# Performance work log

Measured on AMD Instinct MI355X. Metric: run time of the kernel, lower is better.

## Reference

```python
import math
import jax, jax.numpy as jnp
import numpy as np

B, N, D, H, PREFIX = 2, 2048, 2048, 16, 512
HD = D // H
ROPE_BASE = 10000.0

def _rope(x):
    # x: [b, h, n, d]; rotate-half RoPE with positions 0..n-1
    d = x.shape[-1]
    n = x.shape[-2]
    inv_freq = 1.0 / (ROPE_BASE ** (jnp.arange(0, d, 2, dtype=jnp.float32) / d))  # [d/2]
    pos = jnp.arange(n, dtype=jnp.float32)
    freqs = pos[:, None] * inv_freq[None, :]            # [n, d/2]
    cos, sin = jnp.cos(freqs), jnp.sin(freqs)
    x1, x2 = x[..., : d // 2], x[..., d // 2 :]
    return jnp.concatenate([x1 * cos - x2 * sin, x2 * cos + x1 * sin], axis=-1).astype(x.dtype)

def setup_inputs() -> dict:
    key = jax.random.key(0)
    ks = jax.random.split(key, 6)
    x = jax.random.normal(ks[0], (B, N, D), dtype=jnp.float32)
    prefix_k = jax.random.normal(ks[1], (B, H, PREFIX, HD), dtype=jnp.float32)
    prefix_v = jax.random.normal(ks[2], (B, H, PREFIX, HD), dtype=jnp.float32)
    Wqkv = jax.random.normal(ks[3], (D, 3 * D), dtype=jnp.float32) * (D ** -0.5)
    bqkv = jnp.zeros((3 * D,), dtype=jnp.float32)
    Wff = jax.random.normal(ks[4], (D, D), dtype=jnp.float32) * (D ** -0.5)
    bff = jnp.zeros((D,), dtype=jnp.float32)
    # causal mask over current tokens; prefix (cache) columns fully visible
    causal = jnp.tril(jnp.ones((N, N), dtype=jnp.int32))
    mask = jnp.concatenate([jnp.ones((N, PREFIX), dtype=jnp.int32), causal], axis=1)[None, None]  # [1,1,N,N+PREFIX]
    return {"x": x, "mask": mask, "prefix_k": prefix_k, "prefix_v": prefix_v,
            "Wqkv": Wqkv, "bqkv": bqkv, "Wff": Wff, "bff": bff}

def reference(x, mask, prefix_k, prefix_v, Wqkv, bqkv, Wff, bff):
    b, n, d = x.shape
    h = prefix_k.shape[1]
    hd = d // h
    qkv = (x @ Wqkv + bqkv).reshape(b, n, 3, h, hd)      # 'b n (c h d)'
    qkv = jnp.transpose(qkv, (2, 0, 3, 1, 4))            # -> c b h n d
    q, k, v = qkv[0], qkv[1], qkv[2]
    k = jnp.concatenate([prefix_k, k], axis=2)           # [b,h,kt,hd]
    v = jnp.concatenate([prefix_v, v], axis=2)
    next_prefix_kv = jnp.stack([k, v])                   # cached BEFORE rope (as in source)
    q = _rope(q)
    k = _rope(k)
    scores = jnp.einsum('bhqd,bhkd->bhqk', q, k) / math.sqrt(hd)
    scores = jnp.where(mask == 0, jnp.finfo(scores.dtype).min, scores)
    probs = jax.nn.softmax(scores, axis=-1)              # dropout_prob=0.0 -> identity
    attn_o = jnp.einsum('bhqk,bhkd->bhqd', probs, v)
    attn_o = jnp.transpose(attn_o, (0, 2, 1, 3)).reshape(b, n, d)
    return attn_o @ Wff + bff, next_prefix_kv
```

## Files before the change

### kernel.cpp

```cpp
#include <hip/hip_runtime.h>
#include <hip/hip_bf16.h>
#include <stdint.h>

#define TPB 256

using f32x4 = __attribute__((ext_vector_type(4))) float;
using s16x8 = __attribute__((ext_vector_type(8))) short;
using s16x4 = __attribute__((ext_vector_type(4))) short;

__device__ __forceinline__ short f2bf(float f){
  union { float f; uint32_t u; } v; v.f = f;
  uint32_t u = v.u;
  uint32_t r = (u + 0x7fffu + ((u >> 16) & 1u)) >> 16;
  return (short)(uint16_t)r;
}
__device__ __forceinline__ float bf2f(short b){
  union { uint32_t u; float f; } v; v.u = ((uint32_t)(uint16_t)b) << 16;
  return v.f;
}
__device__ __forceinline__ f32x4 mfma16(s16x8 a, s16x8 b, f32x4 c){
  return __builtin_amdgcn_mfma_f32_16x16x32_bf16(a, b, c, 0, 0, 0);
}

#define AS1(p) ((const __attribute__((address_space(1))) void*)(p))
#define AS3(p) ((__attribute__((address_space(3))) void*)(p))

__device__ __forceinline__ void trans64(const float* __restrict__ W, short* __restrict__ WT,
                                        int K, int Nn, int kt, int nt,
                                        float (*ls)[68], int tid){
  const int k0 = kt*64, n0 = nt*64;
#pragma unroll
  for (int i = 0; i < 4; i++){
    const int row = i*16 + (tid >> 4);
    const int c4  = (tid & 15) * 4;
    float4 v = *(const float4*)&W[(size_t)(k0+row)*Nn + n0 + c4];
    ls[row][c4+0] = v.x; ls[row][c4+1] = v.y; ls[row][c4+2] = v.z; ls[row][c4+3] = v.w;
  }
  __syncthreads();
#pragma unroll
  for (int j = 0; j < 2; j++){
    const int nr = j*32 + (tid >> 3);
    const int kc = (tid & 7) * 8;
    s16x8 o;
#pragma unroll
    for (int e = 0; e < 8; e++) o[e] = f2bf(ls[kc+e][nr]);
    *(s16x8*)&WT[(size_t)(n0+nr)*K + k0 + kc] = o;
  }
}

__global__ void k_prep(const float* __restrict__ x, short* __restrict__ xb,
                       const float* __restrict__ Wqkv, short* __restrict__ wqkvT,
                       const float* __restrict__ Wff,  short* __restrict__ wffT){
  __shared__ float ls[64][68];
  const int tid = threadIdx.x;
  const int bid = (int)blockIdx.x;
  if (bid < 4096){
    int i = bid * TPB + tid;
    const float4* s4 = (const float4*)x;
    float4 a = s4[2*i], b = s4[2*i+1];
    s16x8 o;
    o[0]=f2bf(a.x); o[1]=f2bf(a.y); o[2]=f2bf(a.z); o[3]=f2bf(a.w);
    o[4]=f2bf(b.x); o[5]=f2bf(b.y); o[6]=f2bf(b.z); o[7]=f2bf(b.w);
    *(s16x8*)(xb + 8*(size_t)i) = o;
  } else if (bid < 7168){
    const int tb = bid - 4096;
    trans64(Wqkv, wqkvT, 2048, 6144, tb & 31, tb >> 5, ls, tid);
  } else {
    const int tb = bid - 7168;
    trans64(Wff, wffT, 2048, 2048, tb & 31, tb >> 5, ls, tid);
  }
}

template<int EPI>
__global__ void __launch_bounds__(512, 2) k_gemm8(
    const short* __restrict__ A, const short* __restrict__ Bt,
    int Nn, int K,
    const float* __restrict__ bias,
    float* __restrict__ outp,
    float* __restrict__ kvout,
    short* __restrict__ qpre, short* __restrict__ kpre, short* __restrict__ vpre)
{
  __shared__ __align__(16) short As[3][16384];
  __shared__ __align__(16) short Bs[3][8192];
  const int tid = threadIdx.x;
  const int w = tid >> 6, l = tid & 63;
  const int lrow = l & 15, lg = l >> 4;
  const int wm = w >> 1, wn = w & 1;
  const int m0 = blockIdx.x << 8, n0 = blockIdx.y << 7;
  const int NT = K >> 6;

  f32x4 acc[4][4] = {};

#define STAGE_A(slot, t, j) do {                                             \
    int chunk = ((w*4 + (j)) << 6) + l;                                      \
    int row = chunk >> 3, cc = chunk & 7;                                    \
    __builtin_amdgcn_global_load_lds(                                        \
      AS1(A + (size_t)(m0+row)*K + (t)*64 + ((cc ^ (row&7)) << 3)),          \
      AS3(&As[slot][(w*4 + (j)) << 9]), 16, 0, 0);                           \
  } while(0)
#define STAGE_B(slot, t, j) do {                                             \
    int chunk = ((w*2 + (j)) << 6) + l;                                      \
    int row = chunk >> 3, cc = chunk & 7;                                    \
    __builtin_amdgcn_global_load_lds(                                        \
      AS1(Bt + (size_t)(n0+row)*K + (t)*64 + ((cc ^ (row&7)) << 3)),         \
      AS3(&Bs[slot][(w*2 + (j)) << 9]), 16, 0, 0);                           \
  } while(0)

  STAGE_A(0,0,0); STAGE_A(0,0,1); STAGE_A(0,0,2); STAGE_A(0,0,3);
  STAGE_B(0,0,0); STAGE_B(0,0,1);
  STAGE_A(1,1,0); STAGE_A(1,1,1); STAGE_A(1,1,2); STAGE_A(1,1,3);
  STAGE_B(1,1,0); STAGE_B(1,1,1);

  int slot = 0;
  for (int t = 0; t < NT; ++t){
    if (t < NT-1) asm volatile("s_waitcnt vmcnt(6)" ::: "memory");
    else          asm volatile("s_waitcnt vmcnt(0)" ::: "memory");
    __builtin_amdgcn_s_barrier();
    asm volatile("" ::: "memory");
    const int sslot = (slot == 0) ? 2 : slot - 1;
    const bool st = (t+2) < NT;
    const char* ab = (const char*)As[slot];
    const char* bb = (const char*)Bs[slot];

    s16x8 bfr[4][2];
#pragma unroll
    for (int ni = 0; ni < 4; ni++){
      int row = wn*64 + ni*16 + lrow;
#pragma unroll
      for (int ks = 0; ks < 2; ks++)
        bfr[ni][ks] = *(const s16x8*)(bb + row*128 + ((ks*64 + lg*16) ^ ((row&7)<<4)));
    }
    s16x8 af[2][2];
#pragma unroll
    for (int mi = 0; mi < 2; mi++){
      int row = wm*64 + mi*16 + lrow;
#pragma unroll
      for (int ks = 0; ks < 2; ks++)
        af[mi][ks] = *(const s16x8*)(ab + row*128 + ((ks*64 + lg*16) ^ ((row&7)<<4)));
    }
    if (st){ STAGE_A(sslot,t+2,0); STAGE_A(sslot,t+2,1); STAGE_B(sslot,t+2,0); }
    __builtin_amdgcn_s_setprio(1);
#pragma unroll
    for (int ks = 0; ks < 2; ks++)
#pragma unroll
      for (int mi = 0; mi < 2; mi++)
#pragma unroll
        for (int ni = 0; ni < 4; ni++)
          acc[mi][ni] = mfma16(af[mi][ks], bfr[ni][ks], acc[mi][ni]);
    __builtin_amdgcn_s_setprio(0);

    s16x8 af2[2][2];
#pragma unroll
    for (int mi = 0; mi < 2; mi++){
      int row = wm*64 + (mi+2)*16 + lrow;
#pragma unroll
      for (int ks = 0; ks < 2; ks++)
        af2[mi][ks] = *(const s16x8*)(ab + row*128 + ((ks*64 + lg*16) ^ ((row&7)<<4)));
    }
    if (st){ STAGE_A(sslot,t+2,2); STAGE_A(sslot,t+2,3); STAGE_B(sslot,t+2,1); }
    __builtin_amdgcn_s_setprio(1);
#pragma unroll
    for (int ks = 0; ks < 2; ks++)
#pragma unroll
      for (int mi = 0; mi < 2; mi++)
#pragma unroll
        for (int ni = 0; ni < 4; ni++)
          acc[mi+2][ni] = mfma16(af2[mi][ks], bfr[ni][ks], acc[mi+2][ni]);
    __builtin_amdgcn_s_setprio(0);
    slot = (slot == 2) ? 0 : slot + 1;
  }
#undef STAGE_A
#undef STAGE_B

#pragma unroll
  for (int mi = 0; mi < 4; mi++){
#pragma unroll
    for (int ni = 0; ni < 4; ni++){
      const int c  = n0 + wn*64 + ni*16 + lrow;
      const int mb = m0 + wm*64 + mi*16 + lg*4;
      const float bv = bias[c];
      if (EPI == 1){
#pragma unroll
        for (int r = 0; r < 4; r++)
          outp[(size_t)(mb+r)*Nn + c] = acc[mi][ni][r] + bv;
      } else {
        const int s = c >> 11, h = (c >> 7) & 15, tt = c & 127;
#pragma unroll
        for (int r = 0; r < 4; r++){
          const int m = mb + r;
          const int b = m >> 11, n = m & 2047;
          const int bh = b*16 + h;
          const float val = acc[mi][ni][r] + bv;
          if (s == 0){
            qpre[((size_t)bh*2048 + n)*128 + tt] = f2bf(val);
          } else if (s == 1){
            kvout[((size_t)bh*2560 + 512 + n)*128 + tt] = val;
            kpre[((size_t)bh*2048 + n)*128 + tt] = f2bf(val);
          } else {
            kvout[(size_t)(32 + bh)*327680 + (size_t)(512 + n)*128 + tt] = val;
            vpre[((size_t)bh*2048 + n)*128 + tt] = f2bf(val);
          }
        }
      }
    }
  }
}

__global__ void k_pre(const short* __restrict__ kpre, short* __restrict__ kr,
                      const short* __restrict__ vpre, short* __restrict__ vT,
                      const float* __restrict__ pk, float* __restrict__ kvout0,
                      const float* __restrict__ pv, float* __restrict__ kvout1){
  __shared__ float ls[32][129];
  const int tid = threadIdx.x;
  const int bid = (int)blockIdx.x;
  if (bid < 2048){
    int gid = bid * TPB + tid;
    int jb = (gid & 7) * 8; size_t row = gid >> 3;
    int bh = (int)(row >> 11), n = (int)(row & 2047);
    int pos = 512 + n;
    s16x8 v1 = *(const s16x8*)&kpre[row*128 + jb];
    s16x8 v2 = *(const s16x8*)&kpre[row*128 + 64 + jb];
    s16x8 o1, o2;
#pragma unroll
    for (int e = 0; e < 8; e++){
      float invf = __expf((float)(jb + e) * (-9.210340371976184f/64.0f));
      float sn, cs; __sincosf((float)pos * invf, &sn, &cs);
      float x1 = bf2f(v1[e]), x2 = bf2f(v2[e]);
      o1[e] = f2bf(x1*cs - x2*sn);
      o2[e] = f2bf(x2*cs + x1*sn);
    }
    size_t drow = (size_t)bh*2560 + pos;
    *(s16x8*)&kr[drow*128 + jb]      = o1;
    *(s16x8*)&kr[drow*128 + 64 + jb] = o2;
  } else if (bid < 4096){
    int t2 = bid - 2048;
    int bh = t2 >> 6, nt = t2 & 63;
    int n0 = nt*32;
#pragma unroll
    for (int i = 0; i < 16; i++){
      int idx = i*TPB + tid; int p = idx >> 7, t = idx & 127;
      ls[p][t] = bf2f(vpre[((size_t)bh*2048 + n0 + p)*128 + t]);
    }
    __syncthreads();
#pragma unroll
    for (int i = 0; i < 16; i++){
      int idx = i*TPB + tid; int t = idx >> 5, p = idx & 31;
      vT[((size_t)bh*128 + t)*2560 + 512 + n0 + p] = f2bf(ls[p][t]);
    }
  } else if (bid < 4608){
    int gid = (bid - 4096) * TPB + tid;
    int jb = (gid & 7) * 8; size_t row = gid >> 3;
    int bh = (int)(row >> 9), p = (int)(row & 511);
    float4 a1 = *(const float4*)&pk[row*128 + jb];
    float4 a2 = *(const float4*)&pk[row*128 + jb + 4];
    float4 b1 = *(const float4*)&pk[row*128 + 64 + jb];
    float4 b2 = *(const float4*)&pk[row*128 + 64 + jb + 4];
    size_t orow = (size_t)bh*2560 + p;
    *(float4*)&kvout0[orow*128 + jb]          = a1;
    *(float4*)&kvout0[orow*128 + jb + 4]      = a2;
    *(float4*)&kvout0[orow*128 + 64 + jb]     = b1;
    *(float4*)&kvout0[orow*128 + 64 + jb + 4] = b2;
    float x1[8] = {a1.x,a1.y,a1.z,a1.w,a2.x,a2.y,a2.z,a2.w};
    float x2[8] = {b1.x,b1.y,b1.z,b1.w,b2.x,b2.y,b2.z,b2.w};
    s16x8 o1, o2;
#pragma unroll
    for (int e = 0; e < 8; e++){
      float invf = __expf((float)(jb + e) * (-9.210340371976184f/64.0f));
      float sn, cs; __sincosf((float)p * invf, &sn, &cs);
      o1[e] = f2bf(x1[e]*cs - x2[e]*sn);
      o2[e] = f2bf(x2[e]*cs + x1[e]*sn);
    }
    *(s16x8*)&kr[orow*128 + jb]      = o1;
    *(s16x8*)&kr[orow*128 + 64 + jb] = o2;
  } else {
    int t2 = bid - 4608;
    int bh = t2 >> 4, pt = t2 & 15;
    int p0 = pt*32;
#pragma unroll
    for (int i = 0; i < 16; i++){
      int idx = i*TPB + tid; int p = idx >> 7, t = idx & 127;
      float v = pv[((size_t)bh*512 + p0 + p)*128 + t];
      ls[p][t] = v;
      kvout1[((size_t)bh*2560 + p0 + p)*128 + t] = v;
    }
    __syncthreads();
#pragma unroll
    for (int i = 0; i < 16; i++){
      int idx = i*TPB + tid; int t = idx >> 5, p = idx & 31;
      vT[((size_t)bh*128 + t)*2560 + p0 + p] = f2bf(ls[p][t]);
    }
  }
}

__global__ void __launch_bounds__(256, 2) k_attn(
    const short* __restrict__ qr, const short* __restrict__ kr,
    const short* __restrict__ vT, short* __restrict__ attno)
{
  __shared__ short Ks[2][64*128];
  __shared__ short VTs[2][128*64];
  __shared__ short Ps[4][32*64];
  const int bh = blockIdx.x;
  const int qt = 15 - (int)blockIdx.y;
  const int n = 10 + 2*qt;
  const int tid = threadIdx.x, w = tid >> 6, l = tid & 63;
  const int lrow = l & 15, lg = l >> 4;
  const int b = bh >> 4, h = bh & 15;
  const int qbw = qt*128 + w*32;

  s16x8 qf[2][4];
  {
    const float sc = 0.088388347648318447f * 1.4426950408889634f;
#pragma unroll
    for (int qb = 0; qb < 2; qb++){
      const int nr = qbw + qb*16 + lrow;
      const size_t rr = (size_t)bh*2048 + nr;
#pragma unroll
      for (int ks = 0; ks < 4; ks++)
        qf[qb][ks] = *(const s16x8*)&qr[rr*128 + ks*32 + lg*8];
#pragma unroll
      for (int ks = 0; ks < 2; ks++){
#pragma unroll
        for (int e = 0; e < 8; e++){
          const int j = ks*32 + lg*8 + e;
          const float invf = __expf((float)j * (-9.210340371976184f/64.0f));
          float sn, cs;
          __sincosf((float)nr * invf, &sn, &cs);
          float x1 = bf2f(qf[qb][ks][e]), x2 = bf2f(qf[qb][ks+2][e]);
          qf[qb][ks][e]   = f2bf((x1*cs - x2*sn) * sc);
          qf[qb][ks+2][e] = f2bf((x2*cs + x1*sn) * sc);
        }
      }
    }
  }

#define STAGE_KV(buf, kv0s) do {                                                    \
    _Pragma("unroll")                                                               \
    for (int i_ = 0; i_ < 4; i_++){                                                 \
      int chunk = i_*256 + tid;                                                     \
      int row = chunk >> 4, cc = (chunk & 15) ^ (row & 7);                          \
      __builtin_amdgcn_global_load_lds(                                             \
        AS1(kr + ((size_t)bh*2560 + (kv0s) + row)*128 + cc*8),                      \
        AS3((char*)Ks[buf] + (i_*256 + w*64)*16), 16, 0, 0);                        \
    }                                                                               \
    _Pragma("unroll")                                                               \
    for (int i_ = 0; i_ < 4; i_++){                                                 \
      int chunk = i_*256 + tid;                                                     \
      int row = chunk >> 3, cc = (chunk & 7) ^ (row & 7);                           \
      __builtin_amdgcn_global_load_lds(                                             \
        AS1(vT + ((size_t)bh*128 + row)*2560 + (kv0s) + cc*8),                      \
        AS3((char*)VTs[buf] + (i_*256 + w*64)*16), 16, 0, 0);                       \
    }                                                                               \
  } while(0)

  STAGE_KV(0, 0);
  STAGE_KV(1, 64);

  char* psw = (char*)&Ps[w][0];
  f32x4 acc0[8] = {}, acc1[8] = {};
  float mr0 = -1e30f, ls0 = 0.f;
  float mr1 = -1e30f, ls1 = 0.f;

  for (int t = 0; t < n; t++){
    if (t+1 < n) asm volatile("s_waitcnt vmcnt(8)" ::: "memory");
    else         asm volatile("s_waitcnt vmcnt(0)" ::: "memory");
    __builtin_amdgcn_s_barrier();
    asm volatile("" ::: "memory");
    const char* kb_ = (const char*)Ks[t&1];
    const char* vb_ = (const char*)VTs[t&1];
    const int kv0 = t*64;

    f32x4 sf0[4], sf1[4];
    __builtin_amdgcn_s_setprio(1);
#pragma unroll
    for (int kb = 0; kb < 4; kb++){
      f32x4 s0 = {0.f,0.f,0.f,0.f}, s1 = {0.f,0.f,0.f,0.f};
#pragma unroll
      for (int ks = 0; ks < 4; ks++){
        int row  = kb*16 + lrow;
        int colb = ks*64 + lg*16;
        s16x8 kf = *(const s16x8*)(kb_ + row*256 + (colb ^ ((row&7)<<4)));
        s0 = mfma16(kf, qf[0][ks], s0);
        s1 = mfma16(kf, qf[1][ks], s1);
      }
      sf0[kb] = s0; sf1[kb] = s1;
    }
    __builtin_amdgcn_s_setprio(0);

    if (kv0 + 63 > 512 + qbw){
      const int qme0 = 512 + qbw + lrow;
      const int qme1 = qme0 + 16;
#pragma unroll
      for (int kb = 0; kb < 4; kb++)
#pragma unroll
        for (int r = 0; r < 4; r++){
          int kg = kv0 + kb*16 + lg*4 + r;
          if (kg > qme0) sf0[kb][r] = -1e30f;
          if (kg > qme1) sf1[kb][r] = -1e30f;
        }
    }

    {
      float m_ = fmaxf(
          fmaxf(fmaxf(fmaxf(sf0[0][0],sf0[0][1]),fmaxf(sf0[0][2],sf0[0][3])),
                fmaxf(fmaxf(sf0[1][0],sf0[1][1]),fmaxf(sf0[1][2],sf0[1][3]))),
          fmaxf(fmaxf(fmaxf(sf0[2][0],sf0[2][1]),fmaxf(sf0[2][2],sf0[2][3])),
                fmaxf(fmaxf(sf0[3][0],sf0[3][1]),fmaxf(sf0[3][2],sf0[3][3]))));
      m_ = fmaxf(m_, __shfl_xor(m_, 16));
      m_ = fmaxf(m_, __shfl_xor(m_, 32));
      if (__any(m_ > mr0 + 11.5f)){
        float mnew = fmaxf(mr0, m_);
        float sc = __builtin_amdgcn_exp2f(mr0 - mnew);
        mr0 = mnew; ls0 *= sc;
        float scr[4];
#pragma unroll
        for (int r = 0; r < 4; r++)
          scr[r] = __shfl(sc, (l & 48) | (lg*4 + r));
#pragma unroll
        for (int dt = 0; dt < 8; dt++)
#pragma unroll
          for (int r = 0; r < 4; r++) acc0[dt][r] *= scr[r];
      }
#pragma unroll
      for (int kb = 0; kb < 4; kb++){
        float p0 = __builtin_amdgcn_exp2f(sf0[kb][0] - mr0);
        float p1 = __builtin_amdgcn_exp2f(sf0[kb][1] - mr0);
        float p2 = __builtin_amdgcn_exp2f(sf0[kb][2] - mr0);
        float p3 = __builtin_amdgcn_exp2f(sf0[kb][3] - mr0);
        ls0 += (p0+p1)+(p2+p3);
        s16x4 pk4 = { f2bf(p0), f2bf(p1), f2bf(p2), f2bf(p3) };
        *(s16x4*)(psw + (lrow*128 + ((kb*32 + lg*8) ^ ((lrow&7)<<4)))) = pk4;
      }
    }
    {
      float m_ = fmaxf(
          fmaxf(fmaxf(fmaxf(sf1[0][0],sf1[0][1]),fmaxf(sf1[0][2],sf1[0][3])),
                fmaxf(fmaxf(sf1[1][0],sf1[1][1]),fmaxf(sf1[1][2],sf1[1][3]))),
          fmaxf(fmaxf(fmaxf(sf1[2][0],sf1[2][1]),fmaxf(sf1[2][2],sf1[2][3])),
                fmaxf(fmaxf(sf1[3][0],sf1[3][1]),fmaxf(sf1[3][2],sf1[3][3]))));
      m_ = fmaxf(m_, __shfl_xor(m_, 16));
      m_ = fmaxf(m_, __shfl_xor(m_, 32));
      if (__any(m_ > mr1 + 11.5f)){
        float mnew = fmaxf(mr1, m_);
        float sc = __builtin_amdgcn_exp2f(mr1 - mnew);
        mr1 = mnew; ls1 *= sc;
        float scr[4];
#pragma unroll
        for (int r = 0; r < 4; r++)
          scr[r] = __shfl(sc, (l & 48) | (lg*4 + r));
#pragma unroll
        for (int dt = 0; dt < 8; dt++)
#pragma unroll
          for (int r = 0; r < 4; r++) acc1[dt][r] *= scr[r];
      }
#pragma unroll
      for (int kb = 0; kb < 4; kb++){
        float p0 = __builtin_amdgcn_exp2f(sf1[kb][0] - mr1);
        float p1 = __builtin_amdgcn_exp2f(sf1[kb][1] - mr1);
        float p2 = __builtin_amdgcn_exp2f(sf1[kb][2] - mr1);
        float p3 = __builtin_amdgcn_exp2f(sf1[kb][3] - mr1);
        ls1 += (p0+p1)+(p2+p3);
        s16x4 pk4 = { f2bf(p0), f2bf(p1), f2bf(p2), f2bf(p3) };
        *(s16x4*)(psw + ((16 + lrow)*128 + ((kb*32 + lg*8) ^ ((lrow&7)<<4)))) = pk4;
      }
    }

    __builtin_amdgcn_s_setprio(1);
#pragma unroll
    for (int kp = 0; kp < 2; kp++){
      s16x8 pa0 = *(const s16x8*)(psw + (lrow*128       + ((kp*64 + lg*16) ^ ((lrow&7)<<4))));
      s16x8 pa1 = *(const s16x8*)(psw + ((16+lrow)*128  + ((kp*64 + lg*16) ^ ((lrow&7)<<4))));
#pragma unroll
      for (int dt = 0; dt < 8; dt++){
        int vrow = dt*16 + lrow;
        int vcolb = kp*64 + lg*16;
        s16x8 vf = *(const s16x8*)(vb_ + vrow*128 + (vcolb ^ ((vrow&7)<<4)));
        acc0[dt] = mfma16(pa0, vf, acc0[dt]);
        acc1[dt] = mfma16(pa1, vf, acc1[dt]);
      }
    }
    __builtin_amdgcn_s_setprio(0);

    asm volatile("" ::: "memory");
    __builtin_amdgcn_s_barrier();
    asm volatile("" ::: "memory");
    if (t + 2 < n) STAGE_KV(t&1, (t+2)*64);
  }

  float lsa = ls0;
  lsa += __shfl_xor(lsa, 16);
  lsa += __shfl_xor(lsa, 32);
  float lsb = ls1;
  lsb += __shfl_xor(lsb, 16);
  lsb += __shfl_xor(lsb, 32);
  float linv0[4], linv1[4];
#pragma unroll
  for (int r = 0; r < 4; r++){
    linv0[r] = 1.f / __shfl(lsa, (l & 48) | (lg*4 + r));
    linv1[r] = 1.f / __shfl(lsb, (l & 48) | (lg*4 + r));
  }
  short* lout = (short*)Ks;
#pragma unroll
  for (int dt = 0; dt < 8; dt++){
#pragma unroll
    for (int r = 0; r < 4; r++){
      const int col = dt*16 + lrow;
      lout[(w*32 + lg*4 + r)*128 + col]      = f2bf(acc0[dt][r] * linv0[r]);
      lout[(w*32 + 16 + lg*4 + r)*128 + col] = f2bf(acc1[dt][r] * linv1[r]);
    }
  }
  __syncthreads();
  const size_t gbase = ((size_t)b*2048 + qt*128)*2048 + (size_t)h*128;
#pragma unroll
  for (int i = 0; i < 8; i++){
    const int row = (tid >> 4) + i*16;
    const int chunk = tid & 15;
    s16x8 v = *(const s16x8*)&lout[row*128 + chunk*8];
    *(s16x8*)&attno[gbase + (size_t)row*2048 + chunk*8] = v;
  }
#undef STAGE_KV
}

extern "C" void kernel_launch(void* const* d_in, const int* in_sizes, int n_in,
                              void* d_out, int out_size, void* d_ws, size_t ws_size,
                              hipStream_t stream)
{
  const float* x    = (const float*)d_in[0];
  const float* pk   = (const float*)d_in[2];
  const float* pv   = (const float*)d_in[3];
  const float* Wqkv = (const float*)d_in[4];
  const float* bqkv = (const float*)d_in[5];
  const float* Wff  = (const float*)d_in[6];
  const float* bff  = (const float*)d_in[7];
  float* out   = (float*)d_out;
  float* kvout = out + 8388608;

  char* ws = (char*)d_ws;
  short* xb    = (short*)(ws);
  short* wqkvT = (short*)(ws + 16777216);
  short* wffT  = (short*)(ws + 41943040);
  short* qpre  = (short*)(ws + 50331648);
  short* kpre  = (short*)(ws + 67108864);
  short* vpre  = (short*)(ws + 83886080);
  short* krp   = (short*)(ws + 117440512);
  short* vTp   = (short*)(ws + 138412032);
  short* attno = (short*)(ws + 159383552);

  k_prep<<<8192, TPB, 0, stream>>>(x, xb, Wqkv, wqkvT, Wff, wffT);

  k_gemm8<0><<<dim3(16, 48), 512, 0, stream>>>(xb, wqkvT, 6144, 2048, bqkv,
                                               nullptr, kvout, qpre, kpre, vpre);

  k_pre<<<5120, TPB, 0, stream>>>(kpre, krp, vpre, vTp,
                                  pk, kvout, pv, kvout + (size_t)32*327680);

  k_attn<<<dim3(32, 16), 256, 0, stream>>>(qpre, krp, vTp, attno);

  k_gemm8<1><<<dim3(16, 16), 512, 0, stream>>>(attno, wffT, 2048, 2048, bff,
                                               out, nullptr, nullptr, nullptr, nullptr);
}
```

Before: 297.1 us.

## Fuse K RoPE into QKV GEMM epilogue via LDS-staged coalesced stores

The QKV GEMM epilogue now stages each Q/K tile in shared memory and writes it back with coalesced 16-byte rows. For K it applies RoPE in the epilogue and writes straight into the rotated K buffer. This removes the separate RoPE pass in the follow-up kernel and one bf16 K round trip through global memory. In exchange it adds an LDS barrier and sincos work to the GEMM tail, and reuses the A tile shared memory as scratch.

Result: no change. 297.8 us (+0.2%).

```diff
diff --git a/kernel.cpp b/kernel.cpp
--- a/kernel.cpp
+++ b/kernel.cpp
@@ -172,69 +172,107 @@
 #undef STAGE_A
 #undef STAGE_B
 
-#pragma unroll
-  for (int mi = 0; mi < 4; mi++){
-#pragma unroll
-    for (int ni = 0; ni < 4; ni++){
-      const int c  = n0 + wn*64 + ni*16 + lrow;
-      const int mb = m0 + wm*64 + mi*16 + lg*4;
-      const float bv = bias[c];
-      if (EPI == 1){
+  if (EPI == 1){
+#pragma unroll
+    for (int mi = 0; mi < 4; mi++){
+#pragma unroll
+      for (int ni = 0; ni < 4; ni++){
+        const int c  = n0 + wn*64 + ni*16 + lrow;
+        const int mb = m0 + wm*64 + mi*16 + lg*4;
+        const float bv = bias[c];
 #pragma unroll
         for (int r = 0; r < 4; r++)
           outp[(size_t)(mb+r)*Nn + c] = acc[mi][ni][r] + bv;
-      } else {
-        const int s = c >> 11, h = (c >> 7) & 15, tt = c & 127;
+      }
+    }
+    return;
+  }
+
+  const int sblk = n0 >> 11;
+  const int hblk = (n0 >> 7) & 15;
+  const int bblk = m0 >> 11;
+  const int n0r  = m0 & 2047;
+  const int bhB  = bblk*16 + hblk;
+
+  if (sblk == 2){
+#pragma unroll
+    for (int mi = 0; mi < 4; mi++){
+#pragma unroll
+      for (int ni = 0; ni < 4; ni++){
+        const int tt = wn*64 + ni*16 + lrow;
+        const float bv = bias[n0 + tt];
+        const int mbl = wm*64 + mi*16 + lg*4;
 #pragma unroll
         for (int r = 0; r < 4; r++){
-          const int m = mb + r;
-          const int b = m >> 11, n = m & 2047;
-          const int bh = b*16 + h;
+          const int n = n0r + mbl + r;
           const float val = acc[mi][ni][r] + bv;
-          if (s == 0){
-            qpre[((size_t)bh*2048 + n)*128 + tt] = f2bf(val);
-          } else if (s == 1){
-            kvout[((size_t)bh*2560 + 512 + n)*128 + tt] = val;
-            kpre[((size_t)bh*2048 + n)*128 + tt] = f2bf(val);
-          } else {
-            kvout[(size_t)(32 + bh)*327680 + (size_t)(512 + n)*128 + tt] = val;
-            vpre[((size_t)bh*2048 + n)*128 + tt] = f2bf(val);
-          }
+          kvout[(size_t)(32 + bhB)*327680 + (size_t)(512 + n)*128 + tt] = val;
+          vpre[((size_t)bhB*2048 + n)*128 + tt] = f2bf(val);
         }
       }
     }
-  }
-}
-
-__global__ void k_pre(const short* __restrict__ kpre, short* __restrict__ kr,
-                      const short* __restrict__ vpre, short* __restrict__ vT,
+    return;
+  }
+
+  short* S = (short*)As;
+#pragma unroll
+  for (int mi = 0; mi < 4; mi++){
+#pragma unroll
+    for (int ni = 0; ni < 4; ni++){
+      const int tt = wn*64 + ni*16 + lrow;
+      const float bv = bias[n0 + tt];
+      const int mbl = wm*64 + mi*16 + lg*4;
+#pragma unroll
+      for (int r = 0; r < 4; r++){
+        const float val = acc[mi][ni][r] + bv;
+        if (sblk == 1)
+          kvout[((size_t)bhB*2560 + 512 + n0r + mbl + r)*128 + tt] = val;
+        S[(mbl + r)*136 + tt] = f2bf(val);
+      }
+    }
+  }
+  __syncthreads();
+
+  const int row = tid >> 1;
+  if (sblk == 0){
+    const int jh = (tid & 1) << 6;
+    const size_t gb = ((size_t)bhB*2048 + n0r + row)*128 + jh;
+#pragma unroll
+    for (int u = 0; u < 8; u++)
+      *(s16x8*)&qpre[gb + u*8] = *(const s16x8*)&S[row*136 + jh + u*8];
+  } else {
+    const int jh = (tid & 1) << 5;
+    const int pos = 512 + n0r + row;
+    const size_t gb = ((size_t)bhB*2560 + pos)*128;
+#pragma unroll
+    for (int u = 0; u < 4; u++){
+      s16x8 x1v = *(const s16x8*)&S[row*136 + jh + u*8];
+      s16x8 x2v = *(const s16x8*)&S[row*136 + 64 + jh + u*8];
+      s16x8 o1, o2;
+#pragma unroll
+      for (int e = 0; e < 8; e++){
+        const int j = jh + u*8 + e;
+        const float invf = __expf((float)j * (-9.210340371976184f/64.0f));
+        float sn, cs; __sincosf((float)pos * invf, &sn, &cs);
+        const float x1 = bf2f(x1v[e]), x2 = bf2f(x2v[e]);
+        o1[e] = f2bf(x1*cs - x2*sn);
+        o2[e] = f2bf(x2*cs + x1*sn);
+      }
+      *(s16x8*)&kpre[gb + jh + u*8]      = o1;
+      *(s16x8*)&kpre[gb + 64 + jh + u*8] = o2;
+    }
+  }
+}
+
+__global__ void k_pre(const short* __restrict__ vpre, short* __restrict__ vT,
                       const float* __restrict__ pk, float* __restrict__ kvout0,
+                      short* __restrict__ kr,
                       const float* __restrict__ pv, float* __restrict__ kvout1){
   __shared__ float ls[32][129];
   const int tid = threadIdx.x;
   const int bid = (int)blockIdx.x;
   if (bid < 2048){
-    int gid = bid * TPB + tid;
-    int jb = (gid & 7) * 8; size_t row = gid >> 3;
-    int bh = (int)(row >> 11), n = (int)(row & 2047);
-    int pos = 512 + n;
-    s16x8 v1 = *(const s16x8*)&kpre[row*128 + jb];
-    s16x8 v2 = *(const s16x8*)&kpre[row*128 + 64 + jb];
-    s16x8 o1, o2;
-#pragma unroll
-    for (int e = 0; e < 8; e++){
-      float invf = __expf((float)(jb + e) * (-9.210340371976184f/64.0f));
-      float sn, cs; __sincosf((float)pos * invf, &sn, &cs);
-      float x1 = bf2f(v1[e]), x2 = bf2f(v2[e]);
-      o1[e] = f2bf(x1*cs - x2*sn);
-      o2[e] = f2bf(x2*cs + x1*sn);
-    }
-    size_t drow = (size_t)bh*2560 + pos;
-    *(s16x8*)&kr[drow*128 + jb]      = o1;
-    *(s16x8*)&kr[drow*128 + 64 + jb] = o2;
-  } else if (bid < 4096){
-    int t2 = bid - 2048;
-    int bh = t2 >> 6, nt = t2 & 63;
+    int bh = bid >> 6, nt = bid & 63;
     int n0 = nt*32;
 #pragma unroll
     for (int i = 0; i < 16; i++){
@@ -247,8 +285,8 @@
       int idx = i*TPB + tid; int t = idx >> 5, p = idx & 31;
       vT[((size_t)bh*128 + t)*2560 + 512 + n0 + p] = f2bf(ls[p][t]);
     }
-  } else if (bid < 4608){
-    int gid = (bid - 4096) * TPB + tid;
+  } else if (bid < 2560){
+    int gid = (bid - 2048) * TPB + tid;
     int jb = (gid & 7) * 8; size_t row = gid >> 3;
     int bh = (int)(row >> 9), p = (int)(row & 511);
     float4 a1 = *(const float4*)&pk[row*128 + jb];
@@ -273,7 +311,7 @@
     *(s16x8*)&kr[orow*128 + jb]      = o1;
     *(s16x8*)&kr[orow*128 + 64 + jb] = o2;
   } else {
-    int t2 = bid - 4608;
+    int t2 = bid - 2560;
     int bh = t2 >> 4, pt = t2 & 15;
     int p0 = pt*32;
 #pragma unroll
@@ -539,7 +577,6 @@
   short* wqkvT = (short*)(ws + 16777216);
   short* wffT  = (short*)(ws + 41943040);
   short* qpre  = (short*)(ws + 50331648);
-  short* kpre  = (short*)(ws + 67108864);
   short* vpre  = (short*)(ws + 83886080);
   short* krp   = (short*)(ws + 117440512);
   short* vTp   = (short*)(ws + 138412032);
@@ -548,10 +585,10 @@
   k_prep<<<8192, TPB, 0, stream>>>(x, xb, Wqkv, wqkvT, Wff, wffT);
 
   k_gemm8<0><<<dim3(16, 48), 512, 0, stream>>>(xb, wqkvT, 6144, 2048, bqkv,
-                                               nullptr, kvout, qpre, kpre, vpre);
-
-  k_pre<<<5120, TPB, 0, stream>>>(kpre, krp, vpre, vTp,
-                                  pk, kvout, pv, kvout + (size_t)32*327680);
+                                               nullptr, kvout, qpre, krp, vpre);
+
+  k_pre<<<3072, TPB, 0, stream>>>(vpre, vTp, pk, kvout, krp,
+                                  pv, kvout + (size_t)32*327680);
 
   k_attn<<<dim3(32, 16), 256, 0, stream>>>(qpre, krp, vTp, attno);
 
```
